# Kernel optimization log

Hardware: AMD Instinct MI355X
Metric: run time of the kernel (lower is better)

The kernel has to match this reference:

```python
import jax, jax.numpy as jnp
import numpy as np

B, S, H, L = 64, 512, 768, 32  # batch, seq_len, bert hidden, clauses per doc


def setup_inputs() -> dict:
    key = jax.random.key(0)
    k1, k2, k3, k4 = jax.random.split(key, 4)
    sequence_output = jax.random.normal(k1, (B, S, H), jnp.float32)
    context_h = jax.random.normal(k2, (B, H), jnp.float32)
    # clause boundary positions (SEP indices); pos[0]=0, evenly spaced clauses
    step = (S - 2) // L  # 15 tokens per clause, pos[L]=480 < S-1
    clauses_positions = jnp.tile(jnp.arange(L + 1, dtype=jnp.int32) * step, (B, 1))
    doc_lens = jnp.full((B,), L, dtype=jnp.int32)
    D = 2 * H  # 1536: [clause_mean ; CLS]
    W_pool = jax.random.normal(k3, (D, D), jnp.float32) / np.sqrt(D).astype(np.float32)
    b_pool = jnp.zeros((D,), jnp.float32)
    W_out = jax.random.normal(k4, (D,), jnp.float32) / np.sqrt(D).astype(np.float32)
    b_out = jnp.zeros((), jnp.float32)
    return dict(sequence_output=sequence_output, context_h=context_h,
                W_pool=W_pool, b_pool=b_pool, W_out=W_out, b_out=b_out,
                clauses_positions=clauses_positions, doc_lens=doc_lens)


def reference(sequence_output, context_h, W_pool, b_pool, W_out, b_out,
              clauses_positions, doc_lens):
    # clause i (1..L) covers tokens [pos[i-1]+1, pos[i]]; last clause also
    # includes pos[L]+1 (split_size[-1] += 1 in the torch code).
    starts = clauses_positions[:, :-1] + 1           # [B, L]
    ends = clauses_positions[:, 1:] + 1              # exclusive
    ends = ends.at[:, -1].add(1)                     # last clause gets the SEP
    t = jnp.arange(sequence_output.shape[1])         # [S]
    seg_mask = ((t[None, None, :] >= starts[:, :, None]) &
                (t[None, None, :] < ends[:, :, None]))          # [B, L, S]
    counts = (ends - starts).astype(sequence_output.dtype)      # [B, L]
    sums = jnp.einsum('bls,bsh->blh', seg_mask.astype(sequence_output.dtype),
                      sequence_output)                          # segment sums
    means = sums / counts[:, :, None]                           # [B, L, H]
    cls = jnp.broadcast_to(sequence_output[:, :1, :], means.shape)
    clause_h = jnp.concatenate([means, cls], axis=-1)           # [B, L, 2H]
    pooled = jnp.tanh(clause_h @ W_pool.T + b_pool)             # Pooler
    logits = pooled @ W_out + b_out                             # [B, L]
    return logits
```

## Files before the change

### kernel.cpp

```cpp
#include <hip/hip_runtime.h>
#include <hip/hip_bf16.h>

#define SS 512
#define HH 768
#define LL 32
#define DD 1536
#define MM 2048
#define KA 768
#define NSTEP 12

typedef float f32x4 __attribute__((ext_vector_type(4)));
typedef short bf16x8 __attribute__((ext_vector_type(8)));

__device__ __forceinline__ unsigned short f2bf(float x) {
    union { float f; unsigned u; } v; v.f = x;
    unsigned r = v.u + 0x7fff + ((v.u >> 16) & 1);
    return (unsigned short)(r >> 16);
}

__device__ __forceinline__ void gload16(const unsigned short* g, unsigned short* l) {
    __builtin_amdgcn_global_load_lds(
        (const __attribute__((address_space(1))) void*)g,
        (__attribute__((address_space(3))) void*)l, 16, 0, 0);
}

__global__ __launch_bounds__(256)
void prep(const float* __restrict__ seq, const int* __restrict__ pos,
          const float* __restrict__ Wp, const float* __restrict__ bo,
          unsigned short* __restrict__ Abf, unsigned short* __restrict__ Wbf,
          float* __restrict__ C2, float* __restrict__ out) {
    __shared__ unsigned short CAs[64 * 64];
    __shared__ unsigned short CBs[64 * 64];
    const int blk = blockIdx.x;
    const int tid = threadIdx.x;

    if (blk < 24) {
        const int bcol = blk * 64;
        const int lane = tid & 63;
        const int wid  = tid >> 6;
        const int fr = lane & 15, fq = lane >> 4;
        const int wr = wid >> 1,  wc = wid & 1;
        const int crow = tid >> 2;
        const int cf   = tid & 3;
        const float* gA = seq + (size_t)crow * SS * HH;
        const float* gW = Wp  + (size_t)(bcol + crow) * DD + HH;
        const int s0 = fq ^ (fr & 7);
        const int s1 = s0 ^ 4;
        const int rA = wr * 32 + fr;
        const int rB = wc * 32 + fr;
        const int oA00 = rA * 64 + s0 * 8, oA01 = rA * 64 + s1 * 8;
        const int oA10 = oA00 + 16 * 64,   oA11 = oA01 + 16 * 64;
        const int oB00 = rB * 64 + s0 * 8, oB01 = rB * 64 + s1 * 8;
        const int oB10 = oB00 + 16 * 64,   oB11 = oB01 + 16 * 64;

        f32x4 acc[2][2] = {};
        for (int t = 0; t < NSTEP; ++t) {
            const int k0 = t * 64;
            __syncthreads();
            #pragma unroll
            for (int j = 0; j < 4; ++j) {
                const int f4   = cf + j * 4;
                const int slot = (f4 >> 1) ^ (crow & 7);
                const int off  = crow * 64 + slot * 8 + (f4 & 1) * 4;
                float4 av = *(const float4*)(gA + k0 + f4 * 4);
                float4 wv = *(const float4*)(gW + k0 + f4 * 4);
                ushort4 au, wu;
                au.x = f2bf(av.x); au.y = f2bf(av.y);
                au.z = f2bf(av.z); au.w = f2bf(av.w);
                wu.x = f2bf(wv.x); wu.y = f2bf(wv.y);
                wu.z = f2bf(wv.z); wu.w = f2bf(wv.w);
                *(ushort4*)&CAs[off] = au;
                *(ushort4*)&CBs[off] = wu;
            }
            __syncthreads();
            bf16x8 a00 = *(const bf16x8*)&CAs[oA00];
            bf16x8 a01 = *(const bf16x8*)&CAs[oA01];
            bf16x8 a10 = *(const bf16x8*)&CAs[oA10];
            bf16x8 a11 = *(const bf16x8*)&CAs[oA11];
            bf16x8 b00 = *(const bf16x8*)&CBs[oB00];
            bf16x8 b01 = *(const bf16x8*)&CBs[oB01];
            bf16x8 b10 = *(const bf16x8*)&CBs[oB10];
            bf16x8 b11 = *(const bf16x8*)&CBs[oB11];
            acc[0][0] = __builtin_amdgcn_mfma_f32_16x16x32_bf16(a00, b00, acc[0][0], 0, 0, 0);
            acc[0][0] = __builtin_amdgcn_mfma_f32_16x16x32_bf16(a01, b01, acc[0][0], 0, 0, 0);
            acc[0][1] = __builtin_amdgcn_mfma_f32_16x16x32_bf16(a00, b10, acc[0][1], 0, 0, 0);
            acc[0][1] = __builtin_amdgcn_mfma_f32_16x16x32_bf16(a01, b11, acc[0][1], 0, 0, 0);
            acc[1][0] = __builtin_amdgcn_mfma_f32_16x16x32_bf16(a10, b00, acc[1][0], 0, 0, 0);
            acc[1][0] = __builtin_amdgcn_mfma_f32_16x16x32_bf16(a11, b01, acc[1][0], 0, 0, 0);
            acc[1][1] = __builtin_amdgcn_mfma_f32_16x16x32_bf16(a10, b10, acc[1][1], 0, 0, 0);
            acc[1][1] = __builtin_amdgcn_mfma_f32_16x16x32_bf16(a11, b11, acc[1][1], 0, 0, 0);
        }
        #pragma unroll
        for (int m = 0; m < 2; ++m)
            #pragma unroll
            for (int n = 0; n < 2; ++n) {
                const int col = bcol + wc * 32 + n * 16 + fr;
                #pragma unroll
                for (int r = 0; r < 4; ++r) {
                    const int row = wr * 32 + m * 16 + fq * 4 + r;
                    C2[(size_t)row * DD + col] = acc[m][n][r];
                }
            }
    } else if (blk < 24 + MM) {
        const int row = blk - 24;
        if (tid < 192) {
            const int b = row >> 5;
            const int l = row & 31;
            const int* pb = pos + b * (LL + 1);
            int start = pb[l] + 1;
            int end   = pb[l + 1] + 1;
            if (l == LL - 1) end += 1;
            float inv = 1.0f / (float)(end - start);
            const float* base = seq + (size_t)b * SS * HH;
            float4 a = make_float4(0.f, 0.f, 0.f, 0.f);
            for (int t = start; t < end; ++t) {
                float4 v = reinterpret_cast<const float4*>(base + (size_t)t * HH)[tid];
                a.x += v.x; a.y += v.y; a.z += v.z; a.w += v.w;
            }
            ushort4 m;
            m.x = f2bf(a.x * inv); m.y = f2bf(a.y * inv);
            m.z = f2bf(a.z * inv); m.w = f2bf(a.w * inv);
            reinterpret_cast<ushort4*>(Abf + (size_t)row * KA)[tid] = m;
        }
    } else if (blk < 24 + MM + DD) {
        const int n = blk - 24 - MM;
        if (tid < 192) {
            float4 v = reinterpret_cast<const float4*>(Wp + (size_t)n * DD)[tid];
            ushort4 o;
            o.x = f2bf(v.x); o.y = f2bf(v.y); o.z = f2bf(v.z); o.w = f2bf(v.w);
            reinterpret_cast<ushort4*>(Wbf + (size_t)n * KA)[tid] = o;
        }
    } else {
        const int i = (blk - 24 - MM - DD) * 256 + tid;
        if (i < MM) out[i] = bo[0];
    }
}

__global__ __launch_bounds__(256, 3)
void gemm_mfma(const unsigned short* __restrict__ A,
               const unsigned short* __restrict__ Bm,
               const float* __restrict__ C2g,
               const float* __restrict__ bp,
               const float* __restrict__ Wo,
               float* __restrict__ out) {
    __shared__ unsigned short As[3 * 4096];
    __shared__ unsigned short Bs[3 * 4096];
    const int tid  = threadIdx.x;
    const int wid  = tid >> 6;
    const int lane = tid & 63;
    const int fr   = lane & 15;
    const int fq   = lane >> 4;
    const int wr   = wid >> 1, wc = wid & 1;

    const int blk = blockIdx.x;
    const int c = blk & 7;
    const int i = blk >> 3;
    const int bm = ((c >> 1) << 3) + (i & 7);
    const int bn = (c & 1) * 12 + (i >> 3);
    const int brow = bm * 64;
    const int bcol = bn * 64;

    const int srow = tid >> 3;
    const int sc   = (tid & 7) ^ (srow & 7);
    const unsigned short* gA = A  + (size_t)(brow + srow) * KA + sc * 8;
    const unsigned short* gB = Bm + (size_t)(bcol + srow) * KA + sc * 8;
    unsigned short* asW = As + wid * 512;
    unsigned short* bsW = Bs + wid * 512;

#define STAGE(buf, kt) do {                                          \
        gload16(gA + (kt) * 64,           asW + (buf) * 4096);       \
        gload16(gA + (kt) * 64 + 32 * KA, asW + (buf) * 4096 + 2048);\
        gload16(gB + (kt) * 64,           bsW + (buf) * 4096);       \
        gload16(gB + (kt) * 64 + 32 * KA, bsW + (buf) * 4096 + 2048);\
    } while (0)

    const int s0 = fq ^ (fr & 7);
    const int s1 = s0 ^ 4;
    const int rA = wr * 32 + fr;
    const int rB = wc * 32 + fr;
    const int oA00 = rA * 64 + s0 * 8, oA01 = rA * 64 + s1 * 8;
    const int oA10 = oA00 + 16 * 64,   oA11 = oA01 + 16 * 64;
    const int oB00 = rB * 64 + s0 * 8, oB01 = rB * 64 + s1 * 8;
    const int oB10 = oB00 + 16 * 64,   oB11 = oB01 + 16 * 64;

    f32x4 acc[2][2] = {};

    STAGE(0, 0); STAGE(1, 1);

#define BODY(t, buf) do {                                                     \
        __builtin_amdgcn_sched_barrier(0);                                    \
        if ((t) < NSTEP - 1) asm volatile("s_waitcnt vmcnt(4)" ::: "memory"); \
        else                 asm volatile("s_waitcnt vmcnt(0)" ::: "memory"); \
        __builtin_amdgcn_s_barrier();                                         \
        __builtin_amdgcn_sched_barrier(0);                                    \
        if ((t) + 2 < NSTEP) STAGE(((t) + 2) % 3, (t) + 2);                   \
        const unsigned short* as_ = As + (buf) * 4096;                        \
        const unsigned short* bs_ = Bs + (buf) * 4096;                        \
        bf16x8 a00 = *(const bf16x8*)(as_ + oA00);                            \
        bf16x8 a01 = *(const bf16x8*)(as_ + oA01);                            \
        bf16x8 a10 = *(const bf16x8*)(as_ + oA10);                            \
        bf16x8 a11 = *(const bf16x8*)(as_ + oA11);                            \
        bf16x8 b00 = *(const bf16x8*)(bs_ + oB00);                            \
        bf16x8 b01 = *(const bf16x8*)(bs_ + oB01);                            \
        bf16x8 b10 = *(const bf16x8*)(bs_ + oB10);                            \
        bf16x8 b11 = *(const bf16x8*)(bs_ + oB11);                            \
        __builtin_amdgcn_s_setprio(1);                                        \
        acc[0][0] = __builtin_amdgcn_mfma_f32_16x16x32_bf16(a00, b00, acc[0][0], 0, 0, 0); \
        acc[0][0] = __builtin_amdgcn_mfma_f32_16x16x32_bf16(a01, b01, acc[0][0], 0, 0, 0); \
        acc[0][1] = __builtin_amdgcn_mfma_f32_16x16x32_bf16(a00, b10, acc[0][1], 0, 0, 0); \
        acc[0][1] = __builtin_amdgcn_mfma_f32_16x16x32_bf16(a01, b11, acc[0][1], 0, 0, 0); \
        acc[1][0] = __builtin_amdgcn_mfma_f32_16x16x32_bf16(a10, b00, acc[1][0], 0, 0, 0); \
        acc[1][0] = __builtin_amdgcn_mfma_f32_16x16x32_bf16(a11, b01, acc[1][0], 0, 0, 0); \
        acc[1][1] = __builtin_amdgcn_mfma_f32_16x16x32_bf16(a10, b10, acc[1][1], 0, 0, 0); \
        acc[1][1] = __builtin_amdgcn_mfma_f32_16x16x32_bf16(a11, b11, acc[1][1], 0, 0, 0); \
        __builtin_amdgcn_s_setprio(0);                                        \
    } while (0)

    #pragma unroll
    for (int t = 0; t < NSTEP; ++t) {
        BODY(t, t % 3);
    }
#undef BODY
#undef STAGE

    const float* c2row = C2g + (size_t)(2 * bm + wr) * DD;
    float wo_[2], ad_[2];
    #pragma unroll
    for (int n = 0; n < 2; ++n) {
        const int col = bcol + wc * 32 + n * 16 + fr;
        wo_[n] = Wo[col];
        ad_[n] = bp[col] + c2row[col];
    }
    #pragma unroll
    for (int m = 0; m < 2; ++m) {
        float vsum[4] = {0.f, 0.f, 0.f, 0.f};
        #pragma unroll
        for (int n = 0; n < 2; ++n) {
            #pragma unroll
            for (int r = 0; r < 4; ++r) {
                float x = acc[m][n][r] + ad_[n];
                float th = 1.f - 2.f / (__expf(2.f * x) + 1.f);
                vsum[r] += th * wo_[n];
            }
        }
        #pragma unroll
        for (int r = 0; r < 4; ++r) {
            float v = vsum[r];
            v += __shfl_xor(v, 1, 16);
            v += __shfl_xor(v, 2, 16);
            v += __shfl_xor(v, 4, 16);
            v += __shfl_xor(v, 8, 16);
            if (fr == 0)
                atomicAdd(&out[brow + wr * 32 + m * 16 + fq * 4 + r], v);
        }
    }
}

extern "C" void kernel_launch(void* const* d_in, const int* in_sizes, int n_in,
                              void* d_out, int out_size, void* d_ws, size_t ws_size,
                              hipStream_t stream) {
    const float* seq   = (const float*)d_in[0];
    const float* Wp    = (const float*)d_in[2];
    const float* bp    = (const float*)d_in[3];
    const float* Wo    = (const float*)d_in[4];
    const float* bo    = (const float*)d_in[5];
    const int*   pos   = (const int*)d_in[6];
    float* out = (float*)d_out;

    unsigned short* Abf = (unsigned short*)d_ws;
    unsigned short* Wbf = Abf + (size_t)MM * KA;
    float*          C2  = (float*)(Wbf + (size_t)DD * KA);

    const int grid = 24 + MM + DD + (MM + 255) / 256;
    prep<<<grid, 256, 0, stream>>>(seq, pos, Wp, bo, Abf, Wbf, C2, out);
    gemm_mfma<<<768, 256, 0, stream>>>(Abf, Wbf, C2, bp, Wo, out);
}
```

Baseline: 36.32 us.

## Halve GEMM K-step to 32 and deepen LDS pipeline to six stages

The bf16 MFMA GEMM now walks K in 32-wide steps (24 iterations) instead of 64-wide steps (12), and keeps a six-buffer LDS ring with four stages prefetched instead of three buffers with two. The swizzle and the LDS read offsets are rederived for 32-column rows. The aim is to hide more global-load latency behind compute while keeping total LDS size the same. In exchange there are twice as many barriers and waitcnt points, and fewer MFMAs sit between each sync.

```diff
diff --git a/kernel.cpp b/kernel.cpp
--- a/kernel.cpp
+++ b/kernel.cpp
@@ -7,6 +7,7 @@
 #define DD 1536
 #define MM 2048
 #define KA 768
+#define NST32 24
 #define NSTEP 12
 
 typedef float f32x4 __attribute__((ext_vector_type(4)));
@@ -143,8 +144,8 @@
                const float* __restrict__ bp,
                const float* __restrict__ Wo,
                float* __restrict__ out) {
-    __shared__ unsigned short As[3 * 4096];
-    __shared__ unsigned short Bs[3 * 4096];
+    __shared__ unsigned short As[6 * 2048];
+    __shared__ unsigned short Bs[6 * 2048];
     const int tid  = threadIdx.x;
     const int wid  = tid >> 6;
     const int lane = tid & 63;
@@ -160,65 +161,54 @@
     const int brow = bm * 64;
     const int bcol = bn * 64;
 
-    const int srow = tid >> 3;
-    const int sc   = (tid & 7) ^ (srow & 7);
+    const int srow = tid >> 2;
+    const int sc   = (tid & 3) ^ ((tid >> 3) & 3);
     const unsigned short* gA = A  + (size_t)(brow + srow) * KA + sc * 8;
     const unsigned short* gB = Bm + (size_t)(bcol + srow) * KA + sc * 8;
     unsigned short* asW = As + wid * 512;
     unsigned short* bsW = Bs + wid * 512;
 
-#define STAGE(buf, kt) do {                                          \
-        gload16(gA + (kt) * 64,           asW + (buf) * 4096);       \
-        gload16(gA + (kt) * 64 + 32 * KA, asW + (buf) * 4096 + 2048);\
-        gload16(gB + (kt) * 64,           bsW + (buf) * 4096);       \
-        gload16(gB + (kt) * 64 + 32 * KA, bsW + (buf) * 4096 + 2048);\
+#define STAGE(buf, kt) do {                                \
+        gload16(gA + (kt) * 32, asW + (buf) * 2048);       \
+        gload16(gB + (kt) * 32, bsW + (buf) * 2048);       \
     } while (0)
 
-    const int s0 = fq ^ (fr & 7);
-    const int s1 = s0 ^ 4;
-    const int rA = wr * 32 + fr;
-    const int rB = wc * 32 + fr;
-    const int oA00 = rA * 64 + s0 * 8, oA01 = rA * 64 + s1 * 8;
-    const int oA10 = oA00 + 16 * 64,   oA11 = oA01 + 16 * 64;
-    const int oB00 = rB * 64 + s0 * 8, oB01 = rB * 64 + s1 * 8;
-    const int oB10 = oB00 + 16 * 64,   oB11 = oB01 + 16 * 64;
+    const int sl = fq ^ ((fr >> 1) & 3);
+    const int oA0 = (wr * 32 + fr) * 32 + sl * 8;
+    const int oA1 = oA0 + 16 * 32;
+    const int oB0 = (wc * 32 + fr) * 32 + sl * 8;
+    const int oB1 = oB0 + 16 * 32;
 
     f32x4 acc[2][2] = {};
 
-    STAGE(0, 0); STAGE(1, 1);
+    STAGE(0, 0); STAGE(1, 1); STAGE(2, 2); STAGE(3, 3);
 
 #define BODY(t, buf) do {                                                     \
         __builtin_amdgcn_sched_barrier(0);                                    \
-        if ((t) < NSTEP - 1) asm volatile("s_waitcnt vmcnt(4)" ::: "memory"); \
-        else                 asm volatile("s_waitcnt vmcnt(0)" ::: "memory"); \
+        if ((t) <= 20)      asm volatile("s_waitcnt vmcnt(6)" ::: "memory");  \
+        else if ((t) == 21) asm volatile("s_waitcnt vmcnt(4)" ::: "memory");  \
+        else if ((t) == 22) asm volatile("s_waitcnt vmcnt(2)" ::: "memory");  \
+        else                asm volatile("s_waitcnt vmcnt(0)" ::: "memory");  \
         __builtin_amdgcn_s_barrier();                                         \
         __builtin_amdgcn_sched_barrier(0);                                    \
-        if ((t) + 2 < NSTEP) STAGE(((t) + 2) % 3, (t) + 2);                   \
-        const unsigned short* as_ = As + (buf) * 4096;                        \
-        const unsigned short* bs_ = Bs + (buf) * 4096;                        \
-        bf16x8 a00 = *(const bf16x8*)(as_ + oA00);                            \
-        bf16x8 a01 = *(const bf16x8*)(as_ + oA01);                            \
-        bf16x8 a10 = *(const bf16x8*)(as_ + oA10);                            \
-        bf16x8 a11 = *(const bf16x8*)(as_ + oA11);                            \
-        bf16x8 b00 = *(const bf16x8*)(bs_ + oB00);                            \
-        bf16x8 b01 = *(const bf16x8*)(bs_ + oB01);                            \
-        bf16x8 b10 = *(const bf16x8*)(bs_ + oB10);                            \
-        bf16x8 b11 = *(const bf16x8*)(bs_ + oB11);                            \
+        if ((t) + 4 < NST32) STAGE(((t) + 4) % 6, (t) + 4);                   \
+        const unsigned short* as_ = As + (buf) * 2048;                        \
+        const unsigned short* bs_ = Bs + (buf) * 2048;                        \
+        bf16x8 a0 = *(const bf16x8*)(as_ + oA0);                              \
+        bf16x8 a1 = *(const bf16x8*)(as_ + oA1);                              \
+        bf16x8 b0 = *(const bf16x8*)(bs_ + oB0);                              \
+        bf16x8 b1 = *(const bf16x8*)(bs_ + oB1);                              \
         __builtin_amdgcn_s_setprio(1);                                        \
-        acc[0][0] = __builtin_amdgcn_mfma_f32_16x16x32_bf16(a00, b00, acc[0][0], 0, 0, 0); \
-        acc[0][0] = __builtin_amdgcn_mfma_f32_16x16x32_bf16(a01, b01, acc[0][0], 0, 0, 0); \
-        acc[0][1] = __builtin_amdgcn_mfma_f32_16x16x32_bf16(a00, b10, acc[0][1], 0, 0, 0); \
-        acc[0][1] = __builtin_amdgcn_mfma_f32_16x16x32_bf16(a01, b11, acc[0][1], 0, 0, 0); \
-        acc[1][0] = __builtin_amdgcn_mfma_f32_16x16x32_bf16(a10, b00, acc[1][0], 0, 0, 0); \
-        acc[1][0] = __builtin_amdgcn_mfma_f32_16x16x32_bf16(a11, b01, acc[1][0], 0, 0, 0); \
-        acc[1][1] = __builtin_amdgcn_mfma_f32_16x16x32_bf16(a10, b10, acc[1][1], 0, 0, 0); \
-        acc[1][1] = __builtin_amdgcn_mfma_f32_16x16x32_bf16(a11, b11, acc[1][1], 0, 0, 0); \
+        acc[0][0] = __builtin_amdgcn_mfma_f32_16x16x32_bf16(a0, b0, acc[0][0], 0, 0, 0); \
+        acc[0][1] = __builtin_amdgcn_mfma_f32_16x16x32_bf16(a0, b1, acc[0][1], 0, 0, 0); \
+        acc[1][0] = __builtin_amdgcn_mfma_f32_16x16x32_bf16(a1, b0, acc[1][0], 0, 0, 0); \
+        acc[1][1] = __builtin_amdgcn_mfma_f32_16x16x32_bf16(a1, b1, acc[1][1], 0, 0, 0); \
         __builtin_amdgcn_s_setprio(0);                                        \
     } while (0)
 
     #pragma unroll
-    for (int t = 0; t < NSTEP; ++t) {
-        BODY(t, t % 3);
+    for (int t = 0; t < NST32; ++t) {
+        BODY(t, t % 6);
     }
 #undef BODY
 #undef STAGE
```

Result: slower. 38.83 us (+6.9%).
